# Optimization experiments

Measured on AMD Instinct MI355X. Metric: run time of the kernel, lower is better.

The kernel has to match this reference:

```python
import jax, jax.numpy as jnp
import numpy as np

DIM = 768
NUM_CLASS = 1024
INST_PER_CLASS = 64
BATCH = NUM_CLASS * INST_PER_CLASS  # 65536
MOMENTUM = 0.8
ALPHA = 1.0
EPS = 1e-12  # F.normalize eps


def _l2_normalize(x):
    # F.normalize(x, dim=1): x / max(||x||_2, eps)
    n = jnp.sqrt(jnp.sum(x * x, axis=1, keepdims=True))
    return x / jnp.maximum(n, EPS)


def _ema_update_centers(feat, label, old_centers):
    # segment-mean over classes (compute_center) + EMA scatter write (update1),
    # only rows whose class appears in the batch are updated.
    s = jax.ops.segment_sum(feat, label, num_segments=NUM_CLASS)           # [C, D]
    cnt = jax.ops.segment_sum(jnp.ones((feat.shape[0],), feat.dtype),
                              label, num_segments=NUM_CLASS)               # [C]
    mean = s / jnp.maximum(cnt, 1.0)[:, None]
    present = (cnt > 0)[:, None]
    new = jnp.where(present, MOMENTum_ema(mean, old_centers), old_centers)
    # centers are detached / non-trainable in the original module
    return jax.lax.stop_gradient(new)


def MOMENTum_ema(mean, old):
    return MOMENTUM * mean + (1.0 - MOMENTUM) * old


def setup_inputs() -> dict:
    key = jax.random.key(0)
    ks = jax.random.split(key, 6)
    mk = lambda k: jax.random.normal(k, (BATCH, DIM), dtype=jnp.float32)
    ck = lambda k: 0.02 * jax.random.normal(k, (NUM_CLASS, DIM), dtype=jnp.float32)
    # block-structured labels: 64 contiguous instances per class (as the
    # torch code's chunk/::chunk logic assumes)
    label_ = jnp.repeat(jnp.arange(NUM_CLASS, dtype=jnp.int32), INST_PER_CLASS)
    return {
        "RGB_feat": mk(ks[0]),
        "NIR_feat": mk(ks[1]),
        "TIR_feat": mk(ks[2]),
        "RGB_centers": ck(ks[3]),
        "NIR_centers": ck(ks[4]),
        "TIR_centers": ck(ks[5]),
        "label_": label_,
        "epoch": 5,
    }


def reference(RGB_feat, NIR_feat, TIR_feat,
              RGB_centers, NIR_centers, TIR_centers,
              label_, epoch):
    rgb = _l2_normalize(RGB_feat)
    nir = _l2_normalize(NIR_feat)
    tir = _l2_normalize(TIR_feat)

    # update1: per-class segment mean + EMA scatter into the center tables
    new_r = _ema_update_centers(rgb, label_, RGB_centers)
    new_n = _ema_update_centers(nir, label_, NIR_centers)
    new_t = _ema_update_centers(tir, label_, TIR_centers)

    # compute_inter_loss: with block-structured equal-chunk labels the gathered
    # centers_modality tensor equals centers[label_] row-for-row -> plain MSE.
    def mse_to_center(centers, feat):
        d = centers[label_] - feat  # [B, D] gather
        return jnp.mean(d * d)

    intra = (mse_to_center(new_r, rgb)
             + mse_to_center(new_n, nir)
             + mse_to_center(new_t, tir))
    # (update2 averages the three tables in-place; it does not affect the
    #  returned loss, so it is elided from the functional forward output.)
    return ALPHA * intra
```

## Files before the change

### kernel.cpp

```cpp
#include <hip/hip_runtime.h>

#define DIM   768
#define NCLS  1024
#define INST  64
#define MOM   0.8f

__device__ __forceinline__ float wave_allreduce(float v) {
#pragma unroll
    for (int m = 1; m < 64; m <<= 1) v += __shfl_xor(v, m, 64);
    return v;
}

__global__ __launch_bounds__(256) void fused_class_kernel(
    const float* __restrict__ f0, const float* __restrict__ f1, const float* __restrict__ f2,
    const float* __restrict__ c0, const float* __restrict__ c1, const float* __restrict__ c2,
    const int*   __restrict__ label,
    float*       __restrict__ partial)
{
    const int blk = blockIdx.x;
    const int mod = blockIdx.y;
    const float* __restrict__ feat = (mod == 0) ? f0 : (mod == 1) ? f1 : f2;
    const float* __restrict__ cent = (mod == 0) ? c0 : (mod == 1) ? c1 : c2;

    const int tid  = threadIdx.x;
    const int lane = tid & 63;
    const int wave = tid >> 6;

    __shared__ float lds_sum[4][DIM];
    __shared__ float lds_red[4];

    const int cls = label[blk * INST];

    float4 a0 = make_float4(0.f, 0.f, 0.f, 0.f);
    float4 a1 = make_float4(0.f, 0.f, 0.f, 0.f);
    float4 a2 = make_float4(0.f, 0.f, 0.f, 0.f);

    const float4* base = (const float4*)feat + (size_t)blk * INST * (DIM / 4);

#pragma unroll 2
    for (int j = 0; j < INST / 4; ++j) {
        const int r = wave + 4 * j;
        const float4* row = base + (size_t)r * (DIM / 4);
        const float4 x = row[lane];
        const float4 y = row[lane + 64];
        const float4 z = row[lane + 128];

        float s = x.x * x.x + x.y * x.y + x.z * x.z + x.w * x.w
                + y.x * y.x + y.y * y.y + y.z * y.z + y.w * y.w
                + z.x * z.x + z.y * z.y + z.z * z.z + z.w * z.w;
        s = wave_allreduce(s);
        const float inv = 1.0f / fmaxf(sqrtf(s), 1e-12f);

        a0.x = fmaf(x.x, inv, a0.x); a0.y = fmaf(x.y, inv, a0.y);
        a0.z = fmaf(x.z, inv, a0.z); a0.w = fmaf(x.w, inv, a0.w);
        a1.x = fmaf(y.x, inv, a1.x); a1.y = fmaf(y.y, inv, a1.y);
        a1.z = fmaf(y.z, inv, a1.z); a1.w = fmaf(y.w, inv, a1.w);
        a2.x = fmaf(z.x, inv, a2.x); a2.y = fmaf(z.y, inv, a2.y);
        a2.z = fmaf(z.z, inv, a2.z); a2.w = fmaf(z.w, inv, a2.w);
    }

    float4* dst = (float4*)lds_sum[wave];
    dst[lane]       = a0;
    dst[lane + 64]  = a1;
    dst[lane + 128] = a2;
    __syncthreads();

    float t = 0.f;
#pragma unroll
    for (int k = 0; k < DIM / 256; ++k) {
        const int d = tid + k * 256;
        const float S = lds_sum[0][d] + lds_sum[1][d] + lds_sum[2][d] + lds_sum[3][d];
        const float c = fmaf(MOM / (float)INST, S,
                             (1.0f - MOM) * cent[(size_t)cls * DIM + d]);
        t = fmaf((float)INST * c, c, t);
        t = fmaf(-2.0f * c, S, t);
    }
    t = wave_allreduce(t);
    if (lane == 0) lds_red[wave] = t;
    __syncthreads();
    if (tid == 0)
        partial[(size_t)mod * NCLS + blk] =
            lds_red[0] + lds_red[1] + lds_red[2] + lds_red[3];
}

__global__ __launch_bounds__(1024) void reduce_kernel(
    const float* __restrict__ partial, float* __restrict__ out)
{
    __shared__ float lds[16];
    const int tid = threadIdx.x;
    float t = partial[tid] + partial[tid + 1024] + partial[tid + 2048];
    t = wave_allreduce(t);
    if ((tid & 63) == 0) lds[tid >> 6] = t;
    __syncthreads();
    if (tid == 0) {
        float s = 0.f;
#pragma unroll
        for (int i = 0; i < 16; ++i) s += lds[i];
        const float B = (float)(NCLS * INST);
        out[0] = (s + 3.0f * B) / (B * (float)DIM);
    }
}

extern "C" void kernel_launch(void* const* d_in, const int* in_sizes, int n_in,
                              void* d_out, int out_size, void* d_ws, size_t ws_size,
                              hipStream_t stream)
{
    const float* f0 = (const float*)d_in[0];
    const float* f1 = (const float*)d_in[1];
    const float* f2 = (const float*)d_in[2];
    const float* c0 = (const float*)d_in[3];
    const float* c1 = (const float*)d_in[4];
    const float* c2 = (const float*)d_in[5];
    const int*   lb = (const int*)d_in[6];

    float* partial = (float*)d_ws;

    dim3 grid(NCLS, 3);
    fused_class_kernel<<<grid, 256, 0, stream>>>(f0, f1, f2, c0, c1, c2, lb, partial);
    reduce_kernel<<<1, 1024, 0, stream>>>(partial, (float*)d_out);
}
```

Measured before the change: 511.4 us.

## Fuse modalities per block, prefetch rows, and use DPP wave reductions

Each block now handles all three modalities for one class, using 512 threads (8 waves) instead of a 3D grid of 256-thread blocks. The row loop issues the next row's loads before normalizing the current row, so memory latency overlaps with compute. The shuffle-based wave reductions are replaced with DPP row operations plus a readlane broadcast, which cuts cross-lane cost. In exchange there are fewer blocks, extra LDS, and an added barrier per modality. Because the loop is no longer unrolled, latency hiding now depends on the one-row prefetch.

After: 514.0 us. About the same (+0.5%).

```diff
diff --git a/kernel.cpp b/kernel.cpp
--- a/kernel.cpp
+++ b/kernel.cpp
@@ -5,82 +5,119 @@
 #define INST  64
 #define MOM   0.8f
 
-__device__ __forceinline__ float wave_allreduce(float v) {
-#pragma unroll
-    for (int m = 1; m < 64; m <<= 1) v += __shfl_xor(v, m, 64);
-    return v;
+__device__ __forceinline__ float wave_sum_bcast(float v) {
+#define DPPA(ctrl, rmask)                                                  \
+    v += __int_as_float(__builtin_amdgcn_update_dpp(                        \
+        0, __float_as_int(v), ctrl, rmask, 0xf, true))
+    DPPA(0x111, 0xf);
+    DPPA(0x112, 0xf);
+    DPPA(0x114, 0xf);
+    DPPA(0x118, 0xf);
+    DPPA(0x142, 0xa);
+    DPPA(0x143, 0xc);
+#undef DPPA
+    return __int_as_float(__builtin_amdgcn_readlane(__float_as_int(v), 63));
 }
 
-__global__ __launch_bounds__(256) void fused_class_kernel(
-    const float* __restrict__ f0, const float* __restrict__ f1, const float* __restrict__ f2,
-    const float* __restrict__ c0, const float* __restrict__ c1, const float* __restrict__ c2,
-    const int*   __restrict__ label,
-    float*       __restrict__ partial)
+__device__ __forceinline__ void do_modality(
+    const float4* __restrict__ base,
+    const float*  __restrict__ centc,
+    float* __restrict__ lds_sum,
+    const int tid, const int lane, const int wave,
+    float& tacc)
 {
-    const int blk = blockIdx.x;
-    const int mod = blockIdx.y;
-    const float* __restrict__ feat = (mod == 0) ? f0 : (mod == 1) ? f1 : f2;
-    const float* __restrict__ cent = (mod == 0) ? c0 : (mod == 1) ? c1 : c2;
-
-    const int tid  = threadIdx.x;
-    const int lane = tid & 63;
-    const int wave = tid >> 6;
-
-    __shared__ float lds_sum[4][DIM];
-    __shared__ float lds_red[4];
-
-    const int cls = label[blk * INST];
-
     float4 a0 = make_float4(0.f, 0.f, 0.f, 0.f);
     float4 a1 = make_float4(0.f, 0.f, 0.f, 0.f);
     float4 a2 = make_float4(0.f, 0.f, 0.f, 0.f);
 
-    const float4* base = (const float4*)feat + (size_t)blk * INST * (DIM / 4);
-
-#pragma unroll 2
-    for (int j = 0; j < INST / 4; ++j) {
-        const int r = wave + 4 * j;
-        const float4* row = base + (size_t)r * (DIM / 4);
-        const float4 x = row[lane];
-        const float4 y = row[lane + 64];
-        const float4 z = row[lane + 128];
-
+    auto normacc = [&](const float4 x, const float4 y, const float4 z) {
         float s = x.x * x.x + x.y * x.y + x.z * x.z + x.w * x.w
                 + y.x * y.x + y.y * y.y + y.z * y.z + y.w * y.w
                 + z.x * z.x + z.y * z.y + z.z * z.z + z.w * z.w;
-        s = wave_allreduce(s);
+        s = wave_sum_bcast(s);
         const float inv = 1.0f / fmaxf(sqrtf(s), 1e-12f);
-
         a0.x = fmaf(x.x, inv, a0.x); a0.y = fmaf(x.y, inv, a0.y);
         a0.z = fmaf(x.z, inv, a0.z); a0.w = fmaf(x.w, inv, a0.w);
         a1.x = fmaf(y.x, inv, a1.x); a1.y = fmaf(y.y, inv, a1.y);
         a1.z = fmaf(y.z, inv, a1.z); a1.w = fmaf(y.w, inv, a1.w);
         a2.x = fmaf(z.x, inv, a2.x); a2.y = fmaf(z.y, inv, a2.y);
         a2.z = fmaf(z.z, inv, a2.z); a2.w = fmaf(z.w, inv, a2.w);
+    };
+
+    const float4* rp = base + (size_t)wave * (DIM / 4);
+    float4 x0 = rp[lane], y0 = rp[lane + 64], z0 = rp[lane + 128];
+#pragma unroll 1
+    for (int j = 0; j < 7; ++j) {
+        rp += 8 * (DIM / 4);
+        const float4 x1 = rp[lane];
+        const float4 y1 = rp[lane + 64];
+        const float4 z1 = rp[lane + 128];
+        normacc(x0, y0, z0);
+        x0 = x1; y0 = y1; z0 = z1;
     }
+    normacc(x0, y0, z0);
 
-    float4* dst = (float4*)lds_sum[wave];
+    float4* dst = (float4*)(lds_sum + (size_t)wave * DIM);
     dst[lane]       = a0;
     dst[lane + 64]  = a1;
     dst[lane + 128] = a2;
     __syncthreads();
 
-    float t = 0.f;
+    {
+        const int d = tid;
+        float S = 0.f;
 #pragma unroll
-    for (int k = 0; k < DIM / 256; ++k) {
-        const int d = tid + k * 256;
-        const float S = lds_sum[0][d] + lds_sum[1][d] + lds_sum[2][d] + lds_sum[3][d];
-        const float c = fmaf(MOM / (float)INST, S,
-                             (1.0f - MOM) * cent[(size_t)cls * DIM + d]);
-        t = fmaf((float)INST * c, c, t);
-        t = fmaf(-2.0f * c, S, t);
+        for (int w = 0; w < 8; ++w) S += lds_sum[w * DIM + d];
+        const float c = fmaf(MOM / (float)INST, S, (1.0f - MOM) * centc[d]);
+        tacc = fmaf((float)INST * c, c, tacc);
+        tacc = fmaf(-2.0f * c, S, tacc);
     }
-    t = wave_allreduce(t);
+    if (tid < DIM - 512) {
+        const int d = tid + 512;
+        float S = 0.f;
+#pragma unroll
+        for (int w = 0; w < 8; ++w) S += lds_sum[w * DIM + d];
+        const float c = fmaf(MOM / (float)INST, S, (1.0f - MOM) * centc[d]);
+        tacc = fmaf((float)INST * c, c, tacc);
+        tacc = fmaf(-2.0f * c, S, tacc);
+    }
+    __syncthreads();
+}
+
+__global__ __launch_bounds__(512, 8) void fused_class_kernel(
+    const float* __restrict__ f0, const float* __restrict__ f1, const float* __restrict__ f2,
+    const float* __restrict__ c0, const float* __restrict__ c1, const float* __restrict__ c2,
+    const int*   __restrict__ label,
+    float*       __restrict__ partial)
+{
+    const int blk  = blockIdx.x;
+    const int tid  = threadIdx.x;
+    const int lane = tid & 63;
+    const int wave = tid >> 6;
+
+    __shared__ float lds_sum[8 * DIM];
+    __shared__ float lds_red[8];
+
+    const int    cls     = label[blk * INST];
+    const size_t rowbase = (size_t)blk * INST * (DIM / 4);
+
+    float tacc = 0.f;
+    do_modality((const float4*)f0 + rowbase, c0 + (size_t)cls * DIM,
+                lds_sum, tid, lane, wave, tacc);
+    do_modality((const float4*)f1 + rowbase, c1 + (size_t)cls * DIM,
+                lds_sum, tid, lane, wave, tacc);
+    do_modality((const float4*)f2 + rowbase, c2 + (size_t)cls * DIM,
+                lds_sum, tid, lane, wave, tacc);
+
+    const float t = wave_sum_bcast(tacc);
     if (lane == 0) lds_red[wave] = t;
     __syncthreads();
-    if (tid == 0)
-        partial[(size_t)mod * NCLS + blk] =
-            lds_red[0] + lds_red[1] + lds_red[2] + lds_red[3];
+    if (tid == 0) {
+        float s = 0.f;
+#pragma unroll
+        for (int w = 0; w < 8; ++w) s += lds_red[w];
+        partial[blk] = s;
+    }
 }
 
 __global__ __launch_bounds__(1024) void reduce_kernel(
@@ -88,8 +125,8 @@
 {
     __shared__ float lds[16];
     const int tid = threadIdx.x;
-    float t = partial[tid] + partial[tid + 1024] + partial[tid + 2048];
-    t = wave_allreduce(t);
+    float t = partial[tid];
+    t = wave_sum_bcast(t);
     if ((tid & 63) == 0) lds[tid >> 6] = t;
     __syncthreads();
     if (tid == 0) {
@@ -115,7 +152,6 @@
 
     float* partial = (float*)d_ws;
 
-    dim3 grid(NCLS, 3);
-    fused_class_kernel<<<grid, 256, 0, stream>>>(f0, f1, f2, c0, c1, c2, lb, partial);
+    fused_class_kernel<<<NCLS, 512, 0, stream>>>(f0, f1, f2, c0, c1, c2, lb, partial);
     reduce_kernel<<<1, 1024, 0, stream>>>(partial, (float*)d_out);
 }
```
